# Performance work log

Hardware: AMD Instinct MI355X
Metric: run time of the kernel (lower is better)

Reference implementation:

```python
import jax, jax.numpy as jnp
import numpy as np

B, LQ, LK = 4, 512, 512
DQ, DC, H = 256, 256, 128


def setup_inputs() -> dict:
    key = jax.random.key(0)
    ks = jax.random.split(key, 8)
    s = lambda d: 1.0 / np.sqrt(d)
    return {
        "query": jax.random.normal(ks[0], (B, LQ, DQ), jnp.float32),
        "context": jax.random.normal(ks[1], (B, LK, DC), jnp.float32),
        "Wq": jax.random.uniform(ks[2], (H, DQ), jnp.float32, -s(DQ), s(DQ)),
        "bq": jax.random.uniform(ks[3], (H,), jnp.float32, -s(DQ), s(DQ)),
        "Wc": jax.random.uniform(ks[4], (H, DC), jnp.float32, -s(DC), s(DC)),
        "bc": jax.random.uniform(ks[5], (H,), jnp.float32, -s(DC), s(DC)),
        "Wv": jax.random.uniform(ks[6], (1, H), jnp.float32, -s(H), s(H)),
        "bv": jax.random.uniform(ks[7], (1,), jnp.float32, -s(H), s(H)),
    }


def reference(query, context, Wq, bq, Wc, bc, Wv, bv):
    # [B,Lq,H] and [B,Lk,H]
    qp = jnp.einsum("bqd,hd->bqh", query, Wq) + bq
    cp = jnp.einsum("bkd,hd->bkh", context, Wc) + bc
    # NOTE: original torch code adds context_proj twice (faithful reproduction)
    kk = qp[:, :, None, :] + 2.0 * cp[:, None, :, :]  # [B,Lq,Lk,H]
    scores = jnp.einsum("bqkh,h->bqk", jnp.tanh(kk), Wv[0]) + bv[0]
    attn = jax.nn.softmax(scores, axis=-1)  # softmax over Lk
    return jnp.einsum("bqk,bkd->bqd", attn, context)  # [B,Lq,Dc]
```

## Files before the change

### kernel.cpp

```cpp
#include <hip/hip_runtime.h>

#define B 4
#define LQ 512
#define LK 512
#define DQ 256
#define DC 256
#define H 128


__global__ __launch_bounds__(256) void ca_wt_kernel(
    const float* __restrict__ Wq, const float* __restrict__ Wc,
    float* __restrict__ WqT4, float* __restrict__ WcT4)
{
    const int blk = blockIdx.x;
    const bool is_q = blk < 128;
    const float* __restrict__ src = is_q ? Wq : Wc;
    float* __restrict__ dst = is_q ? WqT4 : WcT4;
    const int idx = ((is_q ? blk : blk - 128) << 8) + threadIdx.x;
    const int h = idx >> 8;
    const int d = idx & 255;
    dst[(((d >> 2) * H + h) << 2) + (d & 3)] = src[idx];
}

__global__ __launch_bounds__(256) void ca_proj_kernel(
    const float* __restrict__ query, const float* __restrict__ context,
    const float* __restrict__ WqT4, const float* __restrict__ WcT4,
    const float* __restrict__ bq, const float* __restrict__ bc,
    float* __restrict__ Eq, float* __restrict__ EcT)
{
    __shared__ float rows[8 * DQ];
    const int t = threadIdx.x;
    const int blk = blockIdx.x;
    const bool is_q = blk < (B * LQ / 8);
    const int row0 = (is_q ? blk : blk - (B * LQ / 8)) * 8;
    const float* __restrict__ src = is_q ? query : context;
    const float4* __restrict__ w4 = (const float4*)(is_q ? WqT4 : WcT4);

    const float* __restrict__ sp = src + (size_t)row0 * DQ;
#pragma unroll
    for (int i = 0; i < 8; ++i) rows[i * 256 + t] = sp[i * 256 + t];
    __syncthreads();

    const int h  = t & 127;
    const int rg = t >> 7;

    float acc0 = 0.f, acc1 = 0.f, acc2 = 0.f, acc3 = 0.f;
#pragma unroll 4
    for (int d4 = 0; d4 < DQ / 4; ++d4) {
        const float4 w  = w4[d4 * H + h];
        const float4 x0 = *(const float4*)&rows[(rg    ) * DQ + d4 * 4];
        const float4 x1 = *(const float4*)&rows[(rg + 2) * DQ + d4 * 4];
        const float4 x2 = *(const float4*)&rows[(rg + 4) * DQ + d4 * 4];
        const float4 x3 = *(const float4*)&rows[(rg + 6) * DQ + d4 * 4];
        acc0 = fmaf(w.x, x0.x, acc0); acc0 = fmaf(w.y, x0.y, acc0);
        acc0 = fmaf(w.z, x0.z, acc0); acc0 = fmaf(w.w, x0.w, acc0);
        acc1 = fmaf(w.x, x1.x, acc1); acc1 = fmaf(w.y, x1.y, acc1);
        acc1 = fmaf(w.z, x1.z, acc1); acc1 = fmaf(w.w, x1.w, acc1);
        acc2 = fmaf(w.x, x2.x, acc2); acc2 = fmaf(w.y, x2.y, acc2);
        acc2 = fmaf(w.z, x2.z, acc2); acc2 = fmaf(w.w, x2.w, acc2);
        acc3 = fmaf(w.x, x3.x, acc3); acc3 = fmaf(w.y, x3.y, acc3);
        acc3 = fmaf(w.z, x3.z, acc3); acc3 = fmaf(w.w, x3.w, acc3);
    }

    const float bias = (is_q ? bq : bc)[h];
    if (is_q) {
        Eq[(size_t)(row0 + rg    ) * H + h] = __expf(2.f * (acc0 + bias));
        Eq[(size_t)(row0 + rg + 2) * H + h] = __expf(2.f * (acc1 + bias));
        Eq[(size_t)(row0 + rg + 4) * H + h] = __expf(2.f * (acc2 + bias));
        Eq[(size_t)(row0 + rg + 6) * H + h] = __expf(2.f * (acc3 + bias));
    } else {
        const float e0 = __expf(4.f * (acc0 + bias));
        const float e1 = __expf(4.f * (acc1 + bias));
        const float e2 = __expf(4.f * (acc2 + bias));
        const float e3 = __expf(4.f * (acc3 + bias));
        int rc = row0 + rg;
        EcT[((size_t)(rc >> 9) * H + h) * LK + (rc & 511)] = e0; rc += 2;
        EcT[((size_t)(rc >> 9) * H + h) * LK + (rc & 511)] = e1; rc += 2;
        EcT[((size_t)(rc >> 9) * H + h) * LK + (rc & 511)] = e2; rc += 2;
        EcT[((size_t)(rc >> 9) * H + h) * LK + (rc & 511)] = e3;
    }
}

__global__ __launch_bounds__(256) void ca_attn_kernel(
    const float* __restrict__ Eq, const float* __restrict__ EcT,
    const float* __restrict__ context, const float* __restrict__ Wv,
    float* __restrict__ out)
{
    __shared__ float eqs[4][H];
    __shared__ float wv[H];
    __shared__ float sc[4][LK];
    __shared__ float inv[4];

    const int t = threadIdx.x;
    const int bq0 = blockIdx.x * 4;
    const int b = bq0 / LQ;

    if (t < H) {
        wv[t] = Wv[t];
#pragma unroll
        for (int g = 0; g < 4; ++g) eqs[g][t] = Eq[(size_t)(bq0 + g) * H + t];
    }
    __syncthreads();

    const float* __restrict__ ecb = EcT + (size_t)b * H * LK;

    float a00 = 0.f, a01 = 0.f, a10 = 0.f, a11 = 0.f;
    float a20 = 0.f, a21 = 0.f, a30 = 0.f, a31 = 0.f;
#pragma unroll 2
    for (int h4 = 0; h4 < H / 4; ++h4) {
        const float4 w  = *(const float4*)&wv[h4 * 4];
        const float4 e0 = *(const float4*)&eqs[0][h4 * 4];
        const float4 e1 = *(const float4*)&eqs[1][h4 * 4];
        const float4 e2 = *(const float4*)&eqs[2][h4 * 4];
        const float4 e3 = *(const float4*)&eqs[3][h4 * 4];
        const float* __restrict__ ep = ecb + (size_t)h4 * 4 * LK + t;
        const float wl[4] = {w.x, w.y, w.z, w.w};
        const float el0[4] = {e0.x, e0.y, e0.z, e0.w};
        const float el1[4] = {e1.x, e1.y, e1.z, e1.w};
        const float el2[4] = {e2.x, e2.y, e2.z, e2.w};
        const float el3[4] = {e3.x, e3.y, e3.z, e3.w};
#pragma unroll
        for (int c = 0; c < 4; ++c) {
            const float ec0 = ep[c * LK];
            const float ec1 = ep[c * LK + 256];
            const float wc = wl[c];
            float r;
            r = __builtin_amdgcn_rcpf(fmaf(el0[c], ec0, 1.f)); a00 = fmaf(wc, r, a00);
            r = __builtin_amdgcn_rcpf(fmaf(el0[c], ec1, 1.f)); a01 = fmaf(wc, r, a01);
            r = __builtin_amdgcn_rcpf(fmaf(el1[c], ec0, 1.f)); a10 = fmaf(wc, r, a10);
            r = __builtin_amdgcn_rcpf(fmaf(el1[c], ec1, 1.f)); a11 = fmaf(wc, r, a11);
            r = __builtin_amdgcn_rcpf(fmaf(el2[c], ec0, 1.f)); a20 = fmaf(wc, r, a20);
            r = __builtin_amdgcn_rcpf(fmaf(el2[c], ec1, 1.f)); a21 = fmaf(wc, r, a21);
            r = __builtin_amdgcn_rcpf(fmaf(el3[c], ec0, 1.f)); a30 = fmaf(wc, r, a30);
            r = __builtin_amdgcn_rcpf(fmaf(el3[c], ec1, 1.f)); a31 = fmaf(wc, r, a31);
        }
    }

    sc[0][t] = -2.f * a00; sc[0][t + 256] = -2.f * a01;
    sc[1][t] = -2.f * a10; sc[1][t + 256] = -2.f * a11;
    sc[2][t] = -2.f * a20; sc[2][t + 256] = -2.f * a21;
    sc[3][t] = -2.f * a30; sc[3][t + 256] = -2.f * a31;
    __syncthreads();

    {
        const int w_id = t >> 6;
        const int lane = t & 63;
        float v[8];
#pragma unroll
        for (int i = 0; i < 8; ++i) v[i] = sc[w_id][lane + 64 * i];
        float m = v[0];
#pragma unroll
        for (int i = 1; i < 8; ++i) m = fmaxf(m, v[i]);
#pragma unroll
        for (int off = 32; off > 0; off >>= 1) m = fmaxf(m, __shfl_xor(m, off));
        float s = 0.f;
#pragma unroll
        for (int i = 0; i < 8; ++i) { v[i] = __expf(v[i] - m); s += v[i]; }
#pragma unroll
        for (int off = 32; off > 0; off >>= 1) s += __shfl_xor(s, off);
#pragma unroll
        for (int i = 0; i < 8; ++i) sc[w_id][lane + 64 * i] = v[i];
        if (lane == 0) inv[w_id] = 1.f / s;
    }
    __syncthreads();

    const float* __restrict__ ctx = context + (size_t)b * LK * DC + t;
    float o0 = 0.f, o1 = 0.f, o2 = 0.f, o3 = 0.f;
#pragma unroll 2
    for (int k = 0; k < LK; k += 4) {
        const float4 p0 = *(const float4*)&sc[0][k];
        const float4 p1 = *(const float4*)&sc[1][k];
        const float4 p2 = *(const float4*)&sc[2][k];
        const float4 p3 = *(const float4*)&sc[3][k];
        const float pl0[4] = {p0.x, p0.y, p0.z, p0.w};
        const float pl1[4] = {p1.x, p1.y, p1.z, p1.w};
        const float pl2[4] = {p2.x, p2.y, p2.z, p2.w};
        const float pl3[4] = {p3.x, p3.y, p3.z, p3.w};
#pragma unroll
        for (int c = 0; c < 4; ++c) {
            const float cv = ctx[(size_t)(k + c) * DC];
            o0 = fmaf(pl0[c], cv, o0);
            o1 = fmaf(pl1[c], cv, o1);
            o2 = fmaf(pl2[c], cv, o2);
            o3 = fmaf(pl3[c], cv, o3);
        }
    }
    out[(size_t)(bq0 + 0) * DC + t] = o0 * inv[0];
    out[(size_t)(bq0 + 1) * DC + t] = o1 * inv[1];
    out[(size_t)(bq0 + 2) * DC + t] = o2 * inv[2];
    out[(size_t)(bq0 + 3) * DC + t] = o3 * inv[3];
}

extern "C" void kernel_launch(void* const* d_in, const int* in_sizes, int n_in,
                              void* d_out, int out_size, void* d_ws, size_t ws_size,
                              hipStream_t stream) {
    const float* query   = (const float*)d_in[0];
    const float* context = (const float*)d_in[1];
    const float* Wq = (const float*)d_in[2];
    const float* bq = (const float*)d_in[3];
    const float* Wc = (const float*)d_in[4];
    const float* bc = (const float*)d_in[5];
    const float* Wv = (const float*)d_in[6];
    const float* bv = (const float*)d_in[7];
    (void)bv;
    float* out = (float*)d_out;

    float* Eq   = (float*)d_ws;
    float* EcT  = Eq  + (size_t)B * LQ * H;
    float* WqT4 = EcT + (size_t)B * H * LK;
    float* WcT4 = WqT4 + (size_t)H * DQ;

    ca_wt_kernel<<<256, 256, 0, stream>>>(Wq, Wc, WqT4, WcT4);
    ca_proj_kernel<<<B * (LQ + LK) / 8, 256, 0, stream>>>(
        query, context, WqT4, WcT4, bq, bc, Eq, EcT);
    ca_attn_kernel<<<B * LQ / 4, 256, 0, stream>>>(Eq, EcT, context, Wv, out);
}
```

Measured before the change: 120.1 us.

## Widen attention blocks to 512 threads with split-K context reduction

The attention kernel now runs 512 threads per block. Each thread computes one key's scores for four queries, and the weighted context sum is split across eight key slices with float4 columns, then reduced through shared memory. Query and Wv values are read straight from global memory instead of being staged in LDS. The projection kernel drops its LDS row staging in favour of direct global float4 loads with a wave-uniform row index. The aim is more parallelism and less per-thread serial work, at the cost of extra LDS for partial sums and an added reduction step.

```diff
diff --git a/kernel.cpp b/kernel.cpp
--- a/kernel.cpp
+++ b/kernel.cpp
@@ -22,13 +22,12 @@
     dst[(((d >> 2) * H + h) << 2) + (d & 3)] = src[idx];
 }
 
-__global__ __launch_bounds__(256) void ca_proj_kernel(
+__global__ __launch_bounds__(256, 4) void ca_proj_kernel(
     const float* __restrict__ query, const float* __restrict__ context,
     const float* __restrict__ WqT4, const float* __restrict__ WcT4,
     const float* __restrict__ bq, const float* __restrict__ bc,
     float* __restrict__ Eq, float* __restrict__ EcT)
 {
-    __shared__ float rows[8 * DQ];
     const int t = threadIdx.x;
     const int blk = blockIdx.x;
     const bool is_q = blk < (B * LQ / 8);
@@ -36,22 +35,22 @@
     const float* __restrict__ src = is_q ? query : context;
     const float4* __restrict__ w4 = (const float4*)(is_q ? WqT4 : WcT4);
 
-    const float* __restrict__ sp = src + (size_t)row0 * DQ;
-#pragma unroll
-    for (int i = 0; i < 8; ++i) rows[i * 256 + t] = sp[i * 256 + t];
-    __syncthreads();
-
-    const int h  = t & 127;
-    const int rg = t >> 7;
+    const int h = t & 127;
+    const int rg = __builtin_amdgcn_readfirstlane(t >> 7);
+
+    const float* __restrict__ x0p = src + (size_t)(row0 + rg    ) * DQ;
+    const float* __restrict__ x1p = src + (size_t)(row0 + rg + 2) * DQ;
+    const float* __restrict__ x2p = src + (size_t)(row0 + rg + 4) * DQ;
+    const float* __restrict__ x3p = src + (size_t)(row0 + rg + 6) * DQ;
 
     float acc0 = 0.f, acc1 = 0.f, acc2 = 0.f, acc3 = 0.f;
 #pragma unroll 4
     for (int d4 = 0; d4 < DQ / 4; ++d4) {
         const float4 w  = w4[d4 * H + h];
-        const float4 x0 = *(const float4*)&rows[(rg    ) * DQ + d4 * 4];
-        const float4 x1 = *(const float4*)&rows[(rg + 2) * DQ + d4 * 4];
-        const float4 x2 = *(const float4*)&rows[(rg + 4) * DQ + d4 * 4];
-        const float4 x3 = *(const float4*)&rows[(rg + 6) * DQ + d4 * 4];
+        const float4 x0 = *(const float4*)(x0p + d4 * 4);
+        const float4 x1 = *(const float4*)(x1p + d4 * 4);
+        const float4 x2 = *(const float4*)(x2p + d4 * 4);
+        const float4 x3 = *(const float4*)(x3p + d4 * 4);
         acc0 = fmaf(w.x, x0.x, acc0); acc0 = fmaf(w.y, x0.y, acc0);
         acc0 = fmaf(w.z, x0.z, acc0); acc0 = fmaf(w.w, x0.w, acc0);
         acc1 = fmaf(w.x, x1.x, acc1); acc1 = fmaf(w.y, x1.y, acc1);
@@ -81,114 +80,117 @@
     }
 }
 
-__global__ __launch_bounds__(256) void ca_attn_kernel(
+__global__ __launch_bounds__(512, 4) void ca_attn_kernel(
     const float* __restrict__ Eq, const float* __restrict__ EcT,
     const float* __restrict__ context, const float* __restrict__ Wv,
     float* __restrict__ out)
 {
-    __shared__ float eqs[4][H];
-    __shared__ float wv[H];
     __shared__ float sc[4][LK];
+    __shared__ float part[8][4][DC];
     __shared__ float inv[4];
 
     const int t = threadIdx.x;
     const int bq0 = blockIdx.x * 4;
     const int b = bq0 / LQ;
 
-    if (t < H) {
-        wv[t] = Wv[t];
-#pragma unroll
-        for (int g = 0; g < 4; ++g) eqs[g][t] = Eq[(size_t)(bq0 + g) * H + t];
-    }
-    __syncthreads();
-
     const float* __restrict__ ecb = EcT + (size_t)b * H * LK;
-
-    float a00 = 0.f, a01 = 0.f, a10 = 0.f, a11 = 0.f;
-    float a20 = 0.f, a21 = 0.f, a30 = 0.f, a31 = 0.f;
-#pragma unroll 2
+    const float* __restrict__ eqb = Eq + (size_t)bq0 * H;
+
+    float a[4] = {0.f, 0.f, 0.f, 0.f};
+#pragma unroll 4
     for (int h4 = 0; h4 < H / 4; ++h4) {
-        const float4 w  = *(const float4*)&wv[h4 * 4];
-        const float4 e0 = *(const float4*)&eqs[0][h4 * 4];
-        const float4 e1 = *(const float4*)&eqs[1][h4 * 4];
-        const float4 e2 = *(const float4*)&eqs[2][h4 * 4];
-        const float4 e3 = *(const float4*)&eqs[3][h4 * 4];
+        const float4 wv = *(const float4*)(Wv  + h4 * 4);
+        float4 q[4];
+#pragma unroll
+        for (int g = 0; g < 4; ++g)
+            q[g] = *(const float4*)(eqb + g * H + h4 * 4);
         const float* __restrict__ ep = ecb + (size_t)h4 * 4 * LK + t;
-        const float wl[4] = {w.x, w.y, w.z, w.w};
-        const float el0[4] = {e0.x, e0.y, e0.z, e0.w};
-        const float el1[4] = {e1.x, e1.y, e1.z, e1.w};
-        const float el2[4] = {e2.x, e2.y, e2.z, e2.w};
-        const float el3[4] = {e3.x, e3.y, e3.z, e3.w};
-#pragma unroll
-        for (int c = 0; c < 4; ++c) {
-            const float ec0 = ep[c * LK];
-            const float ec1 = ep[c * LK + 256];
-            const float wc = wl[c];
-            float r;
-            r = __builtin_amdgcn_rcpf(fmaf(el0[c], ec0, 1.f)); a00 = fmaf(wc, r, a00);
-            r = __builtin_amdgcn_rcpf(fmaf(el0[c], ec1, 1.f)); a01 = fmaf(wc, r, a01);
-            r = __builtin_amdgcn_rcpf(fmaf(el1[c], ec0, 1.f)); a10 = fmaf(wc, r, a10);
-            r = __builtin_amdgcn_rcpf(fmaf(el1[c], ec1, 1.f)); a11 = fmaf(wc, r, a11);
-            r = __builtin_amdgcn_rcpf(fmaf(el2[c], ec0, 1.f)); a20 = fmaf(wc, r, a20);
-            r = __builtin_amdgcn_rcpf(fmaf(el2[c], ec1, 1.f)); a21 = fmaf(wc, r, a21);
-            r = __builtin_amdgcn_rcpf(fmaf(el3[c], ec0, 1.f)); a30 = fmaf(wc, r, a30);
-            r = __builtin_amdgcn_rcpf(fmaf(el3[c], ec1, 1.f)); a31 = fmaf(wc, r, a31);
-        }
-    }
-
-    sc[0][t] = -2.f * a00; sc[0][t + 256] = -2.f * a01;
-    sc[1][t] = -2.f * a10; sc[1][t + 256] = -2.f * a11;
-    sc[2][t] = -2.f * a20; sc[2][t + 256] = -2.f * a21;
-    sc[3][t] = -2.f * a30; sc[3][t + 256] = -2.f * a31;
+        const float e0 = ep[0 * LK];
+        const float e1 = ep[1 * LK];
+        const float e2 = ep[2 * LK];
+        const float e3 = ep[3 * LK];
+        float r;
+#pragma unroll
+        for (int g = 0; g < 4; ++g) {
+            r = __builtin_amdgcn_rcpf(fmaf(q[g].x, e0, 1.f)); a[g] = fmaf(wv.x, r, a[g]);
+            r = __builtin_amdgcn_rcpf(fmaf(q[g].y, e1, 1.f)); a[g] = fmaf(wv.y, r, a[g]);
+            r = __builtin_amdgcn_rcpf(fmaf(q[g].z, e2, 1.f)); a[g] = fmaf(wv.z, r, a[g]);
+            r = __builtin_amdgcn_rcpf(fmaf(q[g].w, e3, 1.f)); a[g] = fmaf(wv.w, r, a[g]);
+        }
+    }
+#pragma unroll
+    for (int g = 0; g < 4; ++g) sc[g][t] = -2.f * a[g];
     __syncthreads();
 
     {
         const int w_id = t >> 6;
         const int lane = t & 63;
-        float v[8];
-#pragma unroll
-        for (int i = 0; i < 8; ++i) v[i] = sc[w_id][lane + 64 * i];
-        float m = v[0];
-#pragma unroll
-        for (int i = 1; i < 8; ++i) m = fmaxf(m, v[i]);
-#pragma unroll
-        for (int off = 32; off > 0; off >>= 1) m = fmaxf(m, __shfl_xor(m, off));
-        float s = 0.f;
-#pragma unroll
-        for (int i = 0; i < 8; ++i) { v[i] = __expf(v[i] - m); s += v[i]; }
-#pragma unroll
-        for (int off = 32; off > 0; off >>= 1) s += __shfl_xor(s, off);
-#pragma unroll
-        for (int i = 0; i < 8; ++i) sc[w_id][lane + 64 * i] = v[i];
-        if (lane == 0) inv[w_id] = 1.f / s;
+        if (w_id < 4) {
+            float v[8];
+#pragma unroll
+            for (int i = 0; i < 8; ++i) v[i] = sc[w_id][lane + 64 * i];
+            float m = v[0];
+#pragma unroll
+            for (int i = 1; i < 8; ++i) m = fmaxf(m, v[i]);
+#pragma unroll
+            for (int off = 32; off > 0; off >>= 1) m = fmaxf(m, __shfl_xor(m, off));
+            float s = 0.f;
+#pragma unroll
+            for (int i = 0; i < 8; ++i) { v[i] = __expf(v[i] - m); s += v[i]; }
+#pragma unroll
+            for (int off = 32; off > 0; off >>= 1) s += __shfl_xor(s, off);
+#pragma unroll
+            for (int i = 0; i < 8; ++i) sc[w_id][lane + 64 * i] = v[i];
+            if (lane == 0) inv[w_id] = 1.f / s;
+        }
     }
     __syncthreads();
 
-    const float* __restrict__ ctx = context + (size_t)b * LK * DC + t;
-    float o0 = 0.f, o1 = 0.f, o2 = 0.f, o3 = 0.f;
+    {
+        const int kh = t >> 6;
+        const int d4 = (t & 63) * 4;
+        const float* __restrict__ ctx = context + (size_t)b * LK * DC + d4;
+        float4 o[4];
+#pragma unroll
+        for (int g = 0; g < 4; ++g) o[g] = make_float4(0.f, 0.f, 0.f, 0.f);
 #pragma unroll 2
-    for (int k = 0; k < LK; k += 4) {
-        const float4 p0 = *(const float4*)&sc[0][k];
-        const float4 p1 = *(const float4*)&sc[1][k];
-        const float4 p2 = *(const float4*)&sc[2][k];
-        const float4 p3 = *(const float4*)&sc[3][k];
-        const float pl0[4] = {p0.x, p0.y, p0.z, p0.w};
-        const float pl1[4] = {p1.x, p1.y, p1.z, p1.w};
-        const float pl2[4] = {p2.x, p2.y, p2.z, p2.w};
-        const float pl3[4] = {p3.x, p3.y, p3.z, p3.w};
-#pragma unroll
-        for (int c = 0; c < 4; ++c) {
-            const float cv = ctx[(size_t)(k + c) * DC];
-            o0 = fmaf(pl0[c], cv, o0);
-            o1 = fmaf(pl1[c], cv, o1);
-            o2 = fmaf(pl2[c], cv, o2);
-            o3 = fmaf(pl3[c], cv, o3);
-        }
-    }
-    out[(size_t)(bq0 + 0) * DC + t] = o0 * inv[0];
-    out[(size_t)(bq0 + 1) * DC + t] = o1 * inv[1];
-    out[(size_t)(bq0 + 2) * DC + t] = o2 * inv[2];
-    out[(size_t)(bq0 + 3) * DC + t] = o3 * inv[3];
+        for (int j = 0; j < 16; ++j) {
+            const int k = kh * 64 + j * 4;
+            float4 p[4];
+#pragma unroll
+            for (int g = 0; g < 4; ++g) p[g] = *(const float4*)&sc[g][k];
+#pragma unroll
+            for (int c = 0; c < 4; ++c) {
+                const float4 cv = *(const float4*)(ctx + (size_t)(k + c) * DC);
+                const float pc[4] = {p[0].x, p[1].x, p[2].x, p[3].x};
+                const float pd[4] = {p[0].y, p[1].y, p[2].y, p[3].y};
+                const float pe[4] = {p[0].z, p[1].z, p[2].z, p[3].z};
+                const float pf[4] = {p[0].w, p[1].w, p[2].w, p[3].w};
+                const float* sel = (c == 0) ? pc : (c == 1) ? pd : (c == 2) ? pe : pf;
+#pragma unroll
+                for (int g = 0; g < 4; ++g) {
+                    o[g].x = fmaf(sel[g], cv.x, o[g].x);
+                    o[g].y = fmaf(sel[g], cv.y, o[g].y);
+                    o[g].z = fmaf(sel[g], cv.z, o[g].z);
+                    o[g].w = fmaf(sel[g], cv.w, o[g].w);
+                }
+            }
+        }
+#pragma unroll
+        for (int g = 0; g < 4; ++g)
+            *(float4*)&part[kh][g][d4] = o[g];
+    }
+    __syncthreads();
+
+    if (t < 256) {
+#pragma unroll
+        for (int g = 0; g < 4; ++g) {
+            float s = 0.f;
+#pragma unroll
+            for (int kh = 0; kh < 8; ++kh) s += part[kh][g][t];
+            out[(size_t)(bq0 + g) * DC + t] = s * inv[g];
+        }
+    }
 }
 
 extern "C" void kernel_launch(void* const* d_in, const int* in_sizes, int n_in,
@@ -213,5 +215,5 @@
     ca_wt_kernel<<<256, 256, 0, stream>>>(Wq, Wc, WqT4, WcT4);
     ca_proj_kernel<<<B * (LQ + LK) / 8, 256, 0, stream>>>(
         query, context, WqT4, WcT4, bq, bc, Eq, EcT);
-    ca_attn_kernel<<<B * LQ / 4, 256, 0, stream>>>(Eq, EcT, context, Wv, out);
-}
+    ca_attn_kernel<<<B * LQ / 4, 512, 0, stream>>>(Eq, EcT, context, Wv, out);
+}
```

Result: faster. 112.6 us (-6.3%).
